# Kernel optimization log

Hardware: AMD Instinct MI355X
Metric: run time of the kernel (lower is better)

## Reference

```python
import jax, jax.numpy as jnp
import numpy as np

BLOCK_SIZE = 256
EMB = 384
HEAD = 64
B = 256
T = 256

def setup_inputs() -> dict:
    key = jax.random.key(0)
    k1, k2, k3, k4 = jax.random.split(key, 4)
    x = jax.random.normal(k1, (B, T, EMB), dtype=jnp.float32)
    # torch Linear(no bias) default init ~ U(-1/sqrt(in), 1/sqrt(in)); use scaled normal
    s = 1.0 / np.sqrt(EMB)
    Wq = jax.random.normal(k2, (EMB, HEAD), dtype=jnp.float32) * s
    Wk = jax.random.normal(k3, (EMB, HEAD), dtype=jnp.float32) * s
    Wv = jax.random.normal(k4, (EMB, HEAD), dtype=jnp.float32) * s
    return {"x": x, "Wq": Wq, "Wk": Wk, "Wv": Wv}

def reference(x, Wq, Wk, Wv):
    Bb, Tt, C = x.shape
    q = jnp.einsum('btc,ch->bth', x, Wq)
    k = jnp.einsum('btc,ch->bth', x, Wk)
    v = jnp.einsum('btc,ch->bth', x, Wv)
    # NOTE: source scales by C**-0.5 where C = embedding dim (384), not head_size
    scores = jnp.einsum('bth,bsh->bts', q, k) * (C ** -0.5)  # [B,T,T]
    causal = jnp.tril(jnp.ones((Tt, Tt), dtype=bool))
    scores = jnp.where(causal, scores, -jnp.inf)
    weights = jax.nn.softmax(scores, axis=-1)
    # dropout is identity in eval mode (reference baseline)
    out = jnp.einsum('bts,bsh->bth', weights, v)
    return out
```

## Files before the change

kernel.cpp:

```cpp
#include <hip/hip_runtime.h>
#include <hip/hip_bf16.h>
#include <cstdint>
#include <cstddef>

#define B_DIM 256
#define T_DIM 256
#define EMB   384
#define HEAD  64

typedef __attribute__((ext_vector_type(8))) short bf16x8;
typedef __attribute__((ext_vector_type(4))) float f32x4;
typedef __attribute__((ext_vector_type(4))) unsigned int u32x4;

__device__ __forceinline__ unsigned short f2bf(float f) {
    union { float f; unsigned int u; } v; v.f = f;
    unsigned int r = v.u + 0x7fffu + ((v.u >> 16) & 1u);
    return (unsigned short)(r >> 16);
}

__device__ __forceinline__ unsigned int pkbf(float a, float b) {
#if __has_builtin(__builtin_amdgcn_cvt_pk_bf16_f32)
    typedef __attribute__((ext_vector_type(2))) __bf16 bf16x2_t;
    bf16x2_t r = __builtin_amdgcn_cvt_pk_bf16_f32(a, b);
    return *(unsigned int*)&r;
#else
    return (unsigned)f2bf(a) | ((unsigned)f2bf(b) << 16);
#endif
}

__global__ void wprep_kernel(const float* __restrict__ Wq, const float* __restrict__ Wk,
                             const float* __restrict__ Wv, unsigned short* __restrict__ Wb) {
    int g = blockIdx.x * blockDim.x + threadIdx.x;
    if (g >= 9216) return;
    int kkstep = g / 1536, rem = g - kkstep * 1536;
    int r = rem >> 3, cs = rem & 7, c = cs ^ (r & 7);
    const float* W = (r < 64) ? Wq : (r < 128) ? Wk : Wv;
    int h = r & 63;
    unsigned short tmp[8];
#pragma unroll
    for (int e = 0; e < 8; ++e) {
        int k = kkstep * 64 + c * 8 + e;
        tmp[e] = f2bf(W[k * HEAD + h]);
    }
    *(u32x4*)(Wb + (size_t)g * 8) = *(u32x4*)tmp;
}

__global__ __launch_bounds__(512, 2) void fused_kernel(const float* __restrict__ x,
                                                       const unsigned short* __restrict__ Wb,
                                                       float* __restrict__ out) {
    __shared__ union SM {
        struct { unsigned short Xs[2][256][72]; unsigned short Ws[2][12288]; } p1;
        struct { unsigned short qs[256][72]; unsigned short ks[256][72];
                 unsigned short vT[64][264]; unsigned short Ps[8][16][72]; } p2;
    } sm;

    const int tid = threadIdx.x;
    const int w = tid >> 6, lane = tid & 63, qd = lane >> 4, l15 = lane & 15;
    const int mh = w >> 1, nh = w & 1;
    const int b = blockIdx.x;
    const float* xb = x + (size_t)b * T_DIM * EMB;
    const int xrow = tid >> 4, xc4 = (tid & 15) << 2;

    f32x4 acc[4][6];
#pragma unroll
    for (int mt = 0; mt < 4; ++mt)
#pragma unroll
        for (int nt = 0; nt < 6; ++nt) acc[mt][nt] = (f32x4){0.f, 0.f, 0.f, 0.f};

    float4 xr[8];
#pragma unroll
    for (int s = 0; s < 3; ++s) {
        int idx = s * 512 + w * 64;
        const unsigned short* gp = Wb + (size_t)(idx + lane) * 8;
        unsigned short* lp = &sm.p1.Ws[0][idx * 8];
        __builtin_amdgcn_global_load_lds(
            (const __attribute__((address_space(1))) unsigned int*)gp,
            (__attribute__((address_space(3))) unsigned int*)lp, 16, 0, 0);
    }
#pragma unroll
    for (int s = 0; s < 8; ++s)
        xr[s] = *(const float4*)(xb + (size_t)(xrow + 32 * s) * EMB + xc4);
#pragma unroll
    for (int s = 0; s < 8; ++s)
        *(uint2*)&sm.p1.Xs[0][xrow + 32 * s][xc4] = make_uint2(pkbf(xr[s].x, xr[s].y), pkbf(xr[s].z, xr[s].w));

    for (int kk = 0; kk < 6; ++kk) {
        __syncthreads();
        if (kk < 5) {
#pragma unroll
            for (int s = 0; s < 3; ++s) {
                int idx = s * 512 + w * 64;
                const unsigned short* gp = Wb + (size_t)((kk + 1) * 1536 + idx + lane) * 8;
                unsigned short* lp = &sm.p1.Ws[(kk + 1) & 1][idx * 8];
                __builtin_amdgcn_global_load_lds(
                    (const __attribute__((address_space(1))) unsigned int*)gp,
                    (__attribute__((address_space(3))) unsigned int*)lp, 16, 0, 0);
            }
#pragma unroll
            for (int s = 0; s < 8; ++s)
                xr[s] = *(const float4*)(xb + (size_t)(xrow + 32 * s) * EMB + (kk + 1) * 64 + xc4);
        }
#pragma unroll
        for (int kb = 0; kb < 2; ++kb) {
            bf16x8 a[4], bb[6];
#pragma unroll
            for (int mt = 0; mt < 4; ++mt)
                a[mt] = *(const bf16x8*)&sm.p1.Xs[kk & 1][64 * mh + 16 * mt + l15][32 * kb + 8 * qd];
#pragma unroll
            for (int nt = 0; nt < 6; ++nt) {
                int n = 96 * nh + 16 * nt + l15;
                bb[nt] = *(const bf16x8*)&sm.p1.Ws[kk & 1][n * 64 + (((4 * kb + qd) ^ (n & 7)) << 3)];
            }
#pragma unroll
            for (int mt = 0; mt < 4; ++mt)
#pragma unroll
                for (int nt = 0; nt < 6; ++nt)
                    acc[mt][nt] = __builtin_amdgcn_mfma_f32_16x16x32_bf16(a[mt], bb[nt], acc[mt][nt], 0, 0, 0);
        }
        if (kk < 5) {
#pragma unroll
            for (int s = 0; s < 8; ++s)
                *(uint2*)&sm.p1.Xs[(kk + 1) & 1][xrow + 32 * s][xc4] =
                    make_uint2(pkbf(xr[s].x, xr[s].y), pkbf(xr[s].z, xr[s].w));
        }
    }
    __syncthreads();

#pragma unroll
    for (int nt = 0; nt < 6; ++nt) {
        int n = 96 * nh + 16 * nt + l15;
        int arr = n >> 6, h = n & 63;
        if (arr == 2) {
#pragma unroll
            for (int mt = 0; mt < 4; ++mt) {
                int tok0 = 64 * mh + 16 * mt + 4 * qd;
                *(uint2*)&sm.p2.vT[h][tok0] = make_uint2(
                    pkbf(acc[mt][nt][0], acc[mt][nt][1]),
                    pkbf(acc[mt][nt][2], acc[mt][nt][3]));
            }
        } else {
#pragma unroll
            for (int mt = 0; mt < 4; ++mt)
#pragma unroll
                for (int reg = 0; reg < 4; ++reg) {
                    int tok = 64 * mh + 16 * mt + 4 * qd + reg;
                    unsigned short val = f2bf(acc[mt][nt][reg]);
                    if (arr == 0) sm.p2.qs[tok][h] = val;
                    else          sm.p2.ks[tok][h] = val;
                }
        }
    }
    __syncthreads();

    const int tiles[2] = { w, 15 - w };
    bf16x8 aq[2][2];
#pragma unroll
    for (int ti = 0; ti < 2; ++ti)
#pragma unroll
        for (int kbi = 0; kbi < 2; ++kbi)
            aq[ti][kbi] = *(const bf16x8*)&sm.p2.qs[16 * tiles[ti] + l15][32 * kbi + 8 * qd];

    f32x4 O[2][4];
    float l[2][4];
#pragma unroll
    for (int ti = 0; ti < 2; ++ti) {
#pragma unroll
        for (int dn = 0; dn < 4; ++dn) O[ti][dn] = (f32x4){0.f, 0.f, 0.f, 0.f};
#pragma unroll
        for (int reg = 0; reg < 4; ++reg) l[ti][reg] = 0.f;
    }

    const float cExp = 1.4426950408889634f / 19.595917942265423f;

#pragma unroll
    for (int ti = 0; ti < 2; ++ti) {
        const int t = tiles[ti];
        for (int jc = 0; jc <= (t >> 2); ++jc) {
            const int ntmax = min(3, t - 4 * jc);
            f32x4 S[4];
#pragma unroll
            for (int nt = 0; nt < 4; ++nt) {
                if (nt <= ntmax) {
                    bf16x8 b0 = *(const bf16x8*)&sm.p2.ks[64 * jc + 16 * nt + l15][8 * qd];
                    bf16x8 b1 = *(const bf16x8*)&sm.p2.ks[64 * jc + 16 * nt + l15][32 + 8 * qd];
                    f32x4 s = __builtin_amdgcn_mfma_f32_16x16x32_bf16(aq[ti][0], b0, (f32x4){0.f,0.f,0.f,0.f}, 0, 0, 0);
                    s = __builtin_amdgcn_mfma_f32_16x16x32_bf16(aq[ti][1], b1, s, 0, 0, 0);
                    S[nt] = s;
                }
            }
#pragma unroll
            for (int nt = 0; nt < 4; ++nt) {
#pragma unroll
                for (int reg = 0; reg < 4; ++reg) {
                    float p = 0.0f;
                    if (nt <= ntmax) {
                        p = exp2f(S[nt][reg] * cExp);
                        if (4 * jc + nt == t && (l15 > 4 * qd + reg)) p = 0.0f;
                    }
                    l[ti][reg] += p;
                    sm.p2.Ps[w][4 * qd + reg][16 * nt + l15] = f2bf(p);
                }
            }
            bf16x8 ap0 = *(const bf16x8*)&sm.p2.Ps[w][l15][8 * qd];
            bf16x8 ap1 = *(const bf16x8*)&sm.p2.Ps[w][l15][32 + 8 * qd];
#pragma unroll
            for (int dn = 0; dn < 4; ++dn) {
                bf16x8 bv0 = *(const bf16x8*)&sm.p2.vT[16 * dn + l15][64 * jc + 8 * qd];
                bf16x8 bv1 = *(const bf16x8*)&sm.p2.vT[16 * dn + l15][64 * jc + 32 + 8 * qd];
                O[ti][dn] = __builtin_amdgcn_mfma_f32_16x16x32_bf16(ap0, bv0, O[ti][dn], 0, 0, 0);
                O[ti][dn] = __builtin_amdgcn_mfma_f32_16x16x32_bf16(ap1, bv1, O[ti][dn], 0, 0, 0);
            }
        }
    }

#pragma unroll
    for (int ti = 0; ti < 2; ++ti) {
#pragma unroll
        for (int reg = 0; reg < 4; ++reg) {
            float s = l[ti][reg];
            s += __shfl_xor(s, 1);
            s += __shfl_xor(s, 2);
            s += __shfl_xor(s, 4);
            s += __shfl_xor(s, 8);
            float inv = 1.0f / s;
            int row = 16 * tiles[ti] + 4 * qd + reg;
            float* dst = out + ((size_t)b * T_DIM + row) * HEAD;
#pragma unroll
            for (int dn = 0; dn < 4; ++dn)
                dst[16 * dn + l15] = O[ti][dn][reg] * inv;
        }
    }
}

extern "C" void kernel_launch(void* const* d_in, const int* in_sizes, int n_in,
                              void* d_out, int out_size, void* d_ws, size_t ws_size,
                              hipStream_t stream) {
    const float* x  = (const float*)d_in[0];
    const float* Wq = (const float*)d_in[1];
    const float* Wk = (const float*)d_in[2];
    const float* Wv = (const float*)d_in[3];
    float* out = (float*)d_out;

    unsigned short* Wb = (unsigned short*)d_ws;

    wprep_kernel<<<36, 256, 0, stream>>>(Wq, Wk, Wv, Wb);
    fused_kernel<<<B_DIM, 512, 0, stream>>>(x, Wb, out);
}
```

Measured before the change: 171.4 us.

## Interleave both query tiles per key chunk and transpose projection MFMA operands

The attention loop now handles both of a wave's query tiles inside a single key-chunk loop. Each chunk's K and V fragments are loaded from LDS once and shared by both tiles, and P gets a separate buffer per tile. The projection MFMA swaps its operands (W as A, X as B), so q and k can be written to LDS as packed 4-element stores instead of scalar stores, while vT now takes scalar stores. Output writes use nontemporal stores. The aim is fewer LDS reads and stores and more independent MFMA work per iteration, at the cost of higher register pressure.

```diff
diff --git a/kernel.cpp b/kernel.cpp
--- a/kernel.cpp
+++ b/kernel.cpp
@@ -51,7 +51,7 @@
     __shared__ union SM {
         struct { unsigned short Xs[2][256][72]; unsigned short Ws[2][12288]; } p1;
         struct { unsigned short qs[256][72]; unsigned short ks[256][72];
-                 unsigned short vT[64][264]; unsigned short Ps[8][16][72]; } p2;
+                 unsigned short vT[64][264]; unsigned short Ps[8][2][16][72]; } p2;
     } sm;
 
     const int tid = threadIdx.x;
@@ -61,11 +61,11 @@
     const float* xb = x + (size_t)b * T_DIM * EMB;
     const int xrow = tid >> 4, xc4 = (tid & 15) << 2;
 
-    f32x4 acc[4][6];
-#pragma unroll
-    for (int mt = 0; mt < 4; ++mt)
-#pragma unroll
-        for (int nt = 0; nt < 6; ++nt) acc[mt][nt] = (f32x4){0.f, 0.f, 0.f, 0.f};
+    f32x4 acc[6][4];
+#pragma unroll
+    for (int ct = 0; ct < 6; ++ct)
+#pragma unroll
+        for (int tt = 0; tt < 4; ++tt) acc[ct][tt] = (f32x4){0.f, 0.f, 0.f, 0.f};
 
     float4 xr[8];
 #pragma unroll
@@ -102,20 +102,20 @@
         }
 #pragma unroll
         for (int kb = 0; kb < 2; ++kb) {
-            bf16x8 a[4], bb[6];
-#pragma unroll
-            for (int mt = 0; mt < 4; ++mt)
-                a[mt] = *(const bf16x8*)&sm.p1.Xs[kk & 1][64 * mh + 16 * mt + l15][32 * kb + 8 * qd];
-#pragma unroll
-            for (int nt = 0; nt < 6; ++nt) {
-                int n = 96 * nh + 16 * nt + l15;
-                bb[nt] = *(const bf16x8*)&sm.p1.Ws[kk & 1][n * 64 + (((4 * kb + qd) ^ (n & 7)) << 3)];
-            }
-#pragma unroll
-            for (int mt = 0; mt < 4; ++mt)
-#pragma unroll
-                for (int nt = 0; nt < 6; ++nt)
-                    acc[mt][nt] = __builtin_amdgcn_mfma_f32_16x16x32_bf16(a[mt], bb[nt], acc[mt][nt], 0, 0, 0);
+            bf16x8 xf[4], wf[6];
+#pragma unroll
+            for (int tt = 0; tt < 4; ++tt)
+                xf[tt] = *(const bf16x8*)&sm.p1.Xs[kk & 1][64 * mh + 16 * tt + l15][32 * kb + 8 * qd];
+#pragma unroll
+            for (int ct = 0; ct < 6; ++ct) {
+                int n = 96 * nh + 16 * ct + l15;
+                wf[ct] = *(const bf16x8*)&sm.p1.Ws[kk & 1][n * 64 + (((4 * kb + qd) ^ (n & 7)) << 3)];
+            }
+#pragma unroll
+            for (int ct = 0; ct < 6; ++ct)
+#pragma unroll
+                for (int tt = 0; tt < 4; ++tt)
+                    acc[ct][tt] = __builtin_amdgcn_mfma_f32_16x16x32_bf16(wf[ct], xf[tt], acc[ct][tt], 0, 0, 0);
         }
         if (kk < 5) {
 #pragma unroll
@@ -127,38 +127,33 @@
     __syncthreads();
 
 #pragma unroll
-    for (int nt = 0; nt < 6; ++nt) {
-        int n = 96 * nh + 16 * nt + l15;
-        int arr = n >> 6, h = n & 63;
-        if (arr == 2) {
-#pragma unroll
-            for (int mt = 0; mt < 4; ++mt) {
-                int tok0 = 64 * mh + 16 * mt + 4 * qd;
-                *(uint2*)&sm.p2.vT[h][tok0] = make_uint2(
-                    pkbf(acc[mt][nt][0], acc[mt][nt][1]),
-                    pkbf(acc[mt][nt][2], acc[mt][nt][3]));
-            }
-        } else {
-#pragma unroll
-            for (int mt = 0; mt < 4; ++mt)
-#pragma unroll
-                for (int reg = 0; reg < 4; ++reg) {
-                    int tok = 64 * mh + 16 * mt + 4 * qd + reg;
-                    unsigned short val = f2bf(acc[mt][nt][reg]);
-                    if (arr == 0) sm.p2.qs[tok][h] = val;
-                    else          sm.p2.ks[tok][h] = val;
-                }
+    for (int ct = 0; ct < 6; ++ct) {
+        int chBase = 96 * nh + 16 * ct;
+        int arr = chBase >> 6;
+        int lch = (chBase & 63) + 4 * qd;
+#pragma unroll
+        for (int tt = 0; tt < 4; ++tt) {
+            int tok = 64 * mh + 16 * tt + l15;
+            uint2 pk2 = make_uint2(pkbf(acc[ct][tt][0], acc[ct][tt][1]),
+                                   pkbf(acc[ct][tt][2], acc[ct][tt][3]));
+            if (arr == 0)      *(uint2*)&sm.p2.qs[tok][lch] = pk2;
+            else if (arr == 1) *(uint2*)&sm.p2.ks[tok][lch] = pk2;
+            else {
+                const unsigned short* pp = (const unsigned short*)&pk2;
+#pragma unroll
+                for (int reg = 0; reg < 4; ++reg) sm.p2.vT[lch + reg][tok] = pp[reg];
+            }
         }
     }
     __syncthreads();
 
-    const int tiles[2] = { w, 15 - w };
-    bf16x8 aq[2][2];
-#pragma unroll
-    for (int ti = 0; ti < 2; ++ti)
-#pragma unroll
-        for (int kbi = 0; kbi < 2; ++kbi)
-            aq[ti][kbi] = *(const bf16x8*)&sm.p2.qs[16 * tiles[ti] + l15][32 * kbi + 8 * qd];
+    const int t0 = w, t1 = 15 - w;
+    bf16x8 aq0[2], aq1[2];
+#pragma unroll
+    for (int kbi = 0; kbi < 2; ++kbi) {
+        aq0[kbi] = *(const bf16x8*)&sm.p2.qs[16 * t0 + l15][32 * kbi + 8 * qd];
+        aq1[kbi] = *(const bf16x8*)&sm.p2.qs[16 * t1 + l15][32 * kbi + 8 * qd];
+    }
 
     f32x4 O[2][4];
     float l[2][4];
@@ -172,47 +167,81 @@
 
     const float cExp = 1.4426950408889634f / 19.595917942265423f;
 
-#pragma unroll
-    for (int ti = 0; ti < 2; ++ti) {
-        const int t = tiles[ti];
-        for (int jc = 0; jc <= (t >> 2); ++jc) {
-            const int ntmax = min(3, t - 4 * jc);
-            f32x4 S[4];
-#pragma unroll
-            for (int nt = 0; nt < 4; ++nt) {
-                if (nt <= ntmax) {
-                    bf16x8 b0 = *(const bf16x8*)&sm.p2.ks[64 * jc + 16 * nt + l15][8 * qd];
-                    bf16x8 b1 = *(const bf16x8*)&sm.p2.ks[64 * jc + 16 * nt + l15][32 + 8 * qd];
-                    f32x4 s = __builtin_amdgcn_mfma_f32_16x16x32_bf16(aq[ti][0], b0, (f32x4){0.f,0.f,0.f,0.f}, 0, 0, 0);
-                    s = __builtin_amdgcn_mfma_f32_16x16x32_bf16(aq[ti][1], b1, s, 0, 0, 0);
-                    S[nt] = s;
-                }
-            }
-#pragma unroll
-            for (int nt = 0; nt < 4; ++nt) {
+    for (int jc = 0; jc < 5; ++jc) {
+        const bool a0 = (4 * jc <= t0), a1 = (4 * jc <= t1);
+        if (!a0 && !a1) continue;
+        const int nm0 = a0 ? min(3, t0 - 4 * jc) : -1;
+        const int nm1 = a1 ? min(3, t1 - 4 * jc) : -1;
+        const int nmx = nm0 > nm1 ? nm0 : nm1;
+
+        bf16x8 kf[4][2];
+#pragma unroll
+        for (int nt = 0; nt < 4; ++nt)
+            if (nt <= nmx) {
+                kf[nt][0] = *(const bf16x8*)&sm.p2.ks[64 * jc + 16 * nt + l15][8 * qd];
+                kf[nt][1] = *(const bf16x8*)&sm.p2.ks[64 * jc + 16 * nt + l15][32 + 8 * qd];
+            }
+        f32x4 S0[4], S1[4];
+#pragma unroll
+        for (int nt = 0; nt < 4; ++nt) {
+            if (nt <= nm0) {
+                f32x4 s = __builtin_amdgcn_mfma_f32_16x16x32_bf16(aq0[0], kf[nt][0], (f32x4){0.f,0.f,0.f,0.f}, 0, 0, 0);
+                S0[nt] = __builtin_amdgcn_mfma_f32_16x16x32_bf16(aq0[1], kf[nt][1], s, 0, 0, 0);
+            }
+            if (nt <= nm1) {
+                f32x4 s = __builtin_amdgcn_mfma_f32_16x16x32_bf16(aq1[0], kf[nt][0], (f32x4){0.f,0.f,0.f,0.f}, 0, 0, 0);
+                S1[nt] = __builtin_amdgcn_mfma_f32_16x16x32_bf16(aq1[1], kf[nt][1], s, 0, 0, 0);
+            }
+        }
+        if (a0) {
+#pragma unroll
+            for (int nt = 0; nt < 4; ++nt)
 #pragma unroll
                 for (int reg = 0; reg < 4; ++reg) {
                     float p = 0.0f;
-                    if (nt <= ntmax) {
-                        p = exp2f(S[nt][reg] * cExp);
-                        if (4 * jc + nt == t && (l15 > 4 * qd + reg)) p = 0.0f;
+                    if (nt <= nm0) {
+                        p = exp2f(S0[nt][reg] * cExp);
+                        if (4 * jc + nt == t0 && (l15 > 4 * qd + reg)) p = 0.0f;
                     }
-                    l[ti][reg] += p;
-                    sm.p2.Ps[w][4 * qd + reg][16 * nt + l15] = f2bf(p);
+                    l[0][reg] += p;
+                    sm.p2.Ps[w][0][4 * qd + reg][16 * nt + l15] = f2bf(p);
                 }
-            }
-            bf16x8 ap0 = *(const bf16x8*)&sm.p2.Ps[w][l15][8 * qd];
-            bf16x8 ap1 = *(const bf16x8*)&sm.p2.Ps[w][l15][32 + 8 * qd];
-#pragma unroll
-            for (int dn = 0; dn < 4; ++dn) {
-                bf16x8 bv0 = *(const bf16x8*)&sm.p2.vT[16 * dn + l15][64 * jc + 8 * qd];
-                bf16x8 bv1 = *(const bf16x8*)&sm.p2.vT[16 * dn + l15][64 * jc + 32 + 8 * qd];
-                O[ti][dn] = __builtin_amdgcn_mfma_f32_16x16x32_bf16(ap0, bv0, O[ti][dn], 0, 0, 0);
-                O[ti][dn] = __builtin_amdgcn_mfma_f32_16x16x32_bf16(ap1, bv1, O[ti][dn], 0, 0, 0);
-            }
-        }
-    }
-
+        }
+        if (a1) {
+#pragma unroll
+            for (int nt = 0; nt < 4; ++nt)
+#pragma unroll
+                for (int reg = 0; reg < 4; ++reg) {
+                    float p = 0.0f;
+                    if (nt <= nm1) {
+                        p = exp2f(S1[nt][reg] * cExp);
+                        if (4 * jc + nt == t1 && (l15 > 4 * qd + reg)) p = 0.0f;
+                    }
+                    l[1][reg] += p;
+                    sm.p2.Ps[w][1][4 * qd + reg][16 * nt + l15] = f2bf(p);
+                }
+        }
+        bf16x8 ap0a, ap0b, ap1a, ap1b;
+        if (a0) { ap0a = *(const bf16x8*)&sm.p2.Ps[w][0][l15][8 * qd];
+                  ap0b = *(const bf16x8*)&sm.p2.Ps[w][0][l15][32 + 8 * qd]; }
+        if (a1) { ap1a = *(const bf16x8*)&sm.p2.Ps[w][1][l15][8 * qd];
+                  ap1b = *(const bf16x8*)&sm.p2.Ps[w][1][l15][32 + 8 * qd]; }
+#pragma unroll
+        for (int dn = 0; dn < 4; ++dn) {
+            bf16x8 bv0 = *(const bf16x8*)&sm.p2.vT[16 * dn + l15][64 * jc + 8 * qd];
+            bf16x8 bv1 = *(const bf16x8*)&sm.p2.vT[16 * dn + l15][64 * jc + 32 + 8 * qd];
+            if (a0) {
+                O[0][dn] = __builtin_amdgcn_mfma_f32_16x16x32_bf16(ap0a, bv0, O[0][dn], 0, 0, 0);
+                O[0][dn] = __builtin_amdgcn_mfma_f32_16x16x32_bf16(ap0b, bv1, O[0][dn], 0, 0, 0);
+            }
+            if (a1) {
+                O[1][dn] = __builtin_amdgcn_mfma_f32_16x16x32_bf16(ap1a, bv0, O[1][dn], 0, 0, 0);
+                O[1][dn] = __builtin_amdgcn_mfma_f32_16x16x32_bf16(ap1b, bv1, O[1][dn], 0, 0, 0);
+            }
+        }
+    }
+
+    const int tiles[2] = { t0, t1 };
 #pragma unroll
     for (int ti = 0; ti < 2; ++ti) {
 #pragma unroll
@@ -227,7 +256,7 @@
             float* dst = out + ((size_t)b * T_DIM + row) * HEAD;
 #pragma unroll
             for (int dn = 0; dn < 4; ++dn)
-                dst[16 * dn + l15] = O[ti][dn][reg] * inv;
+                __builtin_nontemporal_store(O[ti][dn][reg] * inv, dst + 16 * dn + l15);
         }
     }
 }
```

After: 171.9 us. About the same (+0.3%).
